# Kernel tuning notes

Measured on AMD Instinct MI355X. Metric: run time of the kernel, lower is better.

The kernel has to match this reference:

```python
import jax, jax.numpy as jnp
import numpy as np
from jax import lax

B, S, V, E, H, L, LAT = 32, 64, 32000, 128, 512, 2, 64

def setup_inputs() -> dict:
    key = jax.random.key(0)
    ks = jax.random.split(key, 40)
    sc = 0.05
    inputs = jax.random.randint(ks[0], (B, S), 0, V, dtype=jnp.int32)
    lengths = jnp.sort(jax.random.randint(ks[1], (B,), 1, S + 1, dtype=jnp.int32))[::-1]
    lengths = lengths.at[0].set(S)  # enforce_sorted=True, max length == S for static shapes
    d = {
        'inputs': inputs,
        'lengths': lengths,
        'noise': jax.random.normal(ks[2], (L, B, LAT), jnp.float32),
        'embed_table': jax.random.normal(ks[3], (V, E), jnp.float32) * sc,
        'enc_Wm': jax.random.normal(ks[4], (LAT, E), jnp.float32) * sc,
        'enc_bm': jnp.zeros((LAT,), jnp.float32),
        'enc_Wv': jax.random.normal(ks[5], (LAT, E), jnp.float32) * sc,
        'enc_bv': jnp.zeros((LAT,), jnp.float32),
        'W_l2r': jax.random.normal(ks[6], (H, LAT), jnp.float32) * sc,
        'b_l2r': jnp.zeros((H,), jnp.float32),
        'gru_Wih0': jax.random.normal(ks[7], (3 * H, E), jnp.float32) * sc,
        'gru_Whh0': jax.random.normal(ks[8], (3 * H, H), jnp.float32) * sc,
        'gru_bih0': jnp.zeros((3 * H,), jnp.float32),
        'gru_bhh0': jnp.zeros((3 * H,), jnp.float32),
        'gru_Wih1': jax.random.normal(ks[9], (3 * H, H), jnp.float32) * sc,
        'gru_Whh1': jax.random.normal(ks[10], (3 * H, H), jnp.float32) * sc,
        'gru_bih1': jnp.zeros((3 * H,), jnp.float32),
        'gru_bhh1': jnp.zeros((3 * H,), jnp.float32),
        'W_out': jax.random.normal(ks[11], (V, H), jnp.float32) * sc,
        'b_out': jnp.zeros((V,), jnp.float32),
        'logp_W1': jax.random.normal(ks[12], (200, LAT), jnp.float32) * sc,
        'logp_b1': jnp.zeros((200,), jnp.float32),
        'logp_W2': jax.random.normal(ks[13], (100, 200), jnp.float32) * sc,
        'logp_b2': jnp.zeros((100,), jnp.float32),
        'logp_W3': jax.random.normal(ks[14], (1, 100), jnp.float32) * sc,
        'logp_b3': jnp.zeros((1,), jnp.float32),
        'sas_W1': jax.random.normal(ks[15], (200, LAT), jnp.float32) * sc,
        'sas_b1': jnp.zeros((200,), jnp.float32),
        'sas_W2': jax.random.normal(ks[16], (100, 200), jnp.float32) * sc,
        'sas_b2': jnp.zeros((100,), jnp.float32),
        'sas_W3': jax.random.normal(ks[17], (1, 100), jnp.float32) * sc,
        'sas_b3': jnp.zeros((1,), jnp.float32),
    }
    return d

def _gru_layer(x, h0, Wih, Whh, bih, bhh, lengths):
    # x: [B,T,D]; PyTorch GRU gate order: r, z, n. Packed semantics: state frozen
    # and output zero beyond each sample's length.
    T = x.shape[1]
    xW = jnp.einsum('btd,gd->btg', x, Wih) + bih          # [B,T,3H] one big GEMM
    tmask = jnp.arange(T)[:, None] < lengths[None, :]      # [T,B]
    def step(h, inp):
        xw_t, m_t = inp                                    # [B,3H], [B]
        hW = h @ Whh.T + bhh
        xr, xz, xn = jnp.split(xw_t, 3, axis=-1)
        hr, hz, hn = jnp.split(hW, 3, axis=-1)
        r = jax.nn.sigmoid(xr + hr)
        u = jax.nn.sigmoid(xz + hz)
        n = jnp.tanh(xn + r * hn)
        h_new = (1.0 - u) * n + u * h
        m = m_t[:, None]
        h = jnp.where(m, h_new, h)
        out = jnp.where(m, h_new, 0.0)
        return h, out
    hT, outs = lax.scan(step, h0, (xW.transpose(1, 0, 2), tmask))
    return outs.transpose(1, 0, 2), hT                     # [B,T,H], [B,H]

def _mlp3(x, W1, b1, W2, b2, W3, b3):
    h = jax.nn.relu(x @ W1.T + b1)
    h = jax.nn.relu(h @ W2.T + b2)
    return (h @ W3.T + b3).reshape(-1)

def reference(inputs, lengths, noise, embed_table, enc_Wm, enc_bm, enc_Wv, enc_bv,
              W_l2r, b_l2r, gru_Wih0, gru_Whh0, gru_bih0, gru_bhh0,
              gru_Wih1, gru_Whh1, gru_bih1, gru_bhh1, W_out, b_out,
              logp_W1, logp_b1, logp_W2, logp_b2, logp_W3, logp_b3,
              sas_W1, sas_b1, sas_W2, sas_b2, sas_W3, sas_b3):
    emb = embed_table[inputs]                              # [B,S,E] gather
    # ragged masked segment-sum: sum embeddings of tokens with id > 2 per sample
    mask = (inputs > 2)[..., None].astype(emb.dtype)
    vec_frag = jnp.sum(emb * mask, axis=1)                 # [B,E]
    mean = vec_frag @ enc_Wm.T + enc_bm                    # [B,LAT]
    logv = vec_frag @ enc_Wv.T + enc_bv
    std = jnp.exp(0.5 * logv)
    z = noise * std + mean                                 # [L,B,LAT]
    pred_logp = _mlp3(mean, logp_W1, logp_b1, logp_W2, logp_b2, logp_W3, logp_b3)
    pred_sas = _mlp3(mean, sas_W1, sas_b1, sas_W2, sas_b2, sas_W3, sas_b3)
    state = z @ W_l2r.T + b_l2r                            # [L,B,H]
    # decoder: 2-layer GRU (eval mode: no dropout), then vocab projection
    out0, _ = _gru_layer(emb, state[0], gru_Wih0, gru_Whh0, gru_bih0, gru_bhh0, lengths)
    out1, _ = _gru_layer(out0, state[1], gru_Wih1, gru_Whh1, gru_bih1, gru_bhh1, lengths)
    output = out1 @ W_out.T + b_out                        # [B,S,V]
    return (output, mean, std, z, pred_logp, pred_sas)
```

## Files before the change

### kernel.cpp

```cpp
#include <hip/hip_runtime.h>


typedef __attribute__((ext_vector_type(8))) short bf16x8_t;
typedef __attribute__((ext_vector_type(8))) unsigned short u16x8_t;
typedef __attribute__((ext_vector_type(4))) float f32x4_t;
typedef __attribute__((ext_vector_type(8))) _Float16 f16x8_t;
typedef __attribute__((ext_vector_type(4))) unsigned int u32x4_t;

#define AS_AGENT __HIP_MEMORY_SCOPE_AGENT

static __device__ __forceinline__ unsigned short f2bf(float f) {
    unsigned int u = __float_as_uint(f);
    u += 0x7fffu + ((u >> 16) & 1u);
    return (unsigned short)(u >> 16);
}
static __device__ __forceinline__ unsigned short f2h(float f) {
    _Float16 h = (_Float16)f;
    return __builtin_bit_cast(unsigned short, h);
}
static __device__ __forceinline__ float sigmoidf_(float x) {
    return 1.f / (1.f + __expf(-x));
}

__global__ __launch_bounds__(256) void cvt_bf16_kernel(const float* __restrict__ in,
                                                       unsigned short* __restrict__ out, int n4) {
    int stride = gridDim.x * 256;
    for (int i = blockIdx.x * 256 + threadIdx.x; i < n4; i += stride) {
        float4 v = reinterpret_cast<const float4*>(in)[i];
        ushort4 o;
        o.x = f2bf(v.x); o.y = f2bf(v.y); o.z = f2bf(v.z); o.w = f2bf(v.w);
        reinterpret_cast<ushort4*>(out)[i] = o;
    }
}

__global__ __launch_bounds__(128) void embed_kernel(const int* __restrict__ tok,
                                                    const float* __restrict__ table,
                                                    unsigned short* __restrict__ embb,
                                                    float* __restrict__ vf) {
    const int b = blockIdx.x, e = threadIdx.x;
    float acc = 0.f;
    for (int s = 0; s < 64; ++s) {
        int id = tok[b * 64 + s];
        float v = table[(size_t)id * 128 + e];
        embb[(size_t)(b * 64 + s) * 128 + e] = f2bf(v);
        if (id > 2) acc += v;
    }
    vf[b * 128 + e] = acc;
}

__global__ __launch_bounds__(256) void encoder_kernel(
    const float* __restrict__ vf,
    const float* __restrict__ Wm, const float* __restrict__ bm,
    const float* __restrict__ Wv, const float* __restrict__ bv,
    const float* __restrict__ noise,
    const float* __restrict__ Wl2r, const float* __restrict__ bl2r,
    const float* __restrict__ lW1, const float* __restrict__ lb1,
    const float* __restrict__ lW2, const float* __restrict__ lb2,
    const float* __restrict__ lW3, const float* __restrict__ lb3,
    const float* __restrict__ sW1, const float* __restrict__ sb1,
    const float* __restrict__ sW2, const float* __restrict__ sb2,
    const float* __restrict__ sW3, const float* __restrict__ sb3,
    float* __restrict__ o_mean, float* __restrict__ o_std, float* __restrict__ o_z,
    float* __restrict__ o_logp, float* __restrict__ o_sas,
    float* __restrict__ state)
{
    const int b = blockIdx.x, tid = threadIdx.x;
    __shared__ float v_[128], mn[64], sd[64], zz[2][64], hh1[200], hh2[100];
    if (tid < 128) v_[tid] = vf[b * 128 + tid];
    __syncthreads();
    if (tid < 128) {
        int j = tid & 63;
        bool isv = tid >= 64;
        const float* W = (isv ? Wv : Wm) + j * 128;
        float a = isv ? bv[j] : bm[j];
#pragma unroll 4
        for (int k = 0; k < 128; ++k) a = fmaf(v_[k], W[k], a);
        if (!isv) { mn[j] = a; o_mean[b * 64 + j] = a; }
        else      { float s = __expf(0.5f * a); sd[j] = s; o_std[b * 64 + j] = s; }
    }
    __syncthreads();
    if (tid < 128) {
        int l = tid >> 6, j = tid & 63;
        float zv = fmaf(noise[(l * 32 + b) * 64 + j], sd[j], mn[j]);
        zz[l][j] = zv;
        o_z[(l * 32 + b) * 64 + j] = zv;
    }
    __syncthreads();
#pragma unroll
    for (int p = 0; p < 4; ++p) {
        int tt = p * 256 + tid;
        int l = tt >> 9, hd = tt & 511;
        const float* W = Wl2r + hd * 64;
        float a = bl2r[hd];
#pragma unroll 4
        for (int k = 0; k < 64; ++k) a = fmaf(zz[l][k], W[k], a);
        state[(size_t)(l * 32 + b) * 512 + hd] = a;
    }
    if (tid < 200) {
        const float* W = lW1 + tid * 64;
        float a = lb1[tid];
        for (int k = 0; k < 64; ++k) a = fmaf(mn[k], W[k], a);
        hh1[tid] = fmaxf(a, 0.f);
    }
    __syncthreads();
    if (tid < 100) {
        const float* W = lW2 + tid * 200;
        float a = lb2[tid];
        for (int k = 0; k < 200; ++k) a = fmaf(hh1[k], W[k], a);
        hh2[tid] = fmaxf(a, 0.f);
    }
    __syncthreads();
    if (tid == 0) {
        float a = lb3[0];
        for (int k = 0; k < 100; ++k) a = fmaf(hh2[k], lW3[k], a);
        o_logp[b] = a;
    }
    __syncthreads();
    if (tid < 200) {
        const float* W = sW1 + tid * 64;
        float a = sb1[tid];
        for (int k = 0; k < 64; ++k) a = fmaf(mn[k], W[k], a);
        hh1[tid] = fmaxf(a, 0.f);
    }
    __syncthreads();
    if (tid < 100) {
        const float* W = sW2 + tid * 200;
        float a = sb2[tid];
        for (int k = 0; k < 200; ++k) a = fmaf(hh1[k], W[k], a);
        hh2[tid] = fmaxf(a, 0.f);
    }
    __syncthreads();
    if (tid == 0) {
        float a = sb3[0];
        for (int k = 0; k < 100; ++k) a = fmaf(hh2[k], sW3[k], a);
        o_sas[b] = a;
    }
}

__global__ __launch_bounds__(256) void gemm_bt_kernel(
    const unsigned short* __restrict__ A,
    const unsigned short* __restrict__ B,
    const float* __restrict__ bias,
    float* __restrict__ C,
    int M, int N, int K)
{
    __shared__ unsigned short lA[128 * 64];
    __shared__ unsigned short lB[128 * 64];
    const int tid = threadIdx.x;
    const int lane = tid & 63;
    const int wave = tid >> 6;
    const int wm = wave >> 1, wn = wave & 1;
    const int m0 = blockIdx.y * 128, n0 = blockIdx.x * 128;

    f32x4_t acc[4][4];
#pragma unroll
    for (int i = 0; i < 4; ++i)
#pragma unroll
        for (int j = 0; j < 4; ++j) acc[i][j] = (f32x4_t){0.f, 0.f, 0.f, 0.f};

    for (int kt = 0; kt < K; kt += 64) {
#pragma unroll
        for (int p = 0; p < 4; ++p) {
            int g = p * 256 + tid;
            int row = g >> 3, c8 = g & 7;
            int dst = row * 64 + ((c8 ^ (row & 7)) << 3);
            *(u16x8_t*)&lA[dst] = *(const u16x8_t*)(A + (size_t)(m0 + row) * K + kt + (c8 << 3));
            *(u16x8_t*)&lB[dst] = *(const u16x8_t*)(B + (size_t)(n0 + row) * K + kt + (c8 << 3));
        }
        __syncthreads();
#pragma unroll
        for (int kc = 0; kc < 2; ++kc) {
            bf16x8_t af[4], bfr[4];
            int c8 = kc * 4 + (lane >> 4);
#pragma unroll
            for (int i = 0; i < 4; ++i) {
                int ra = wm * 64 + i * 16 + (lane & 15);
                af[i] = *(const bf16x8_t*)&lA[ra * 64 + ((c8 ^ (ra & 7)) << 3)];
                int rb = wn * 64 + i * 16 + (lane & 15);
                bfr[i] = *(const bf16x8_t*)&lB[rb * 64 + ((c8 ^ (rb & 7)) << 3)];
            }
#pragma unroll
            for (int i = 0; i < 4; ++i)
#pragma unroll
                for (int j = 0; j < 4; ++j)
                    acc[i][j] = __builtin_amdgcn_mfma_f32_16x16x32_bf16(af[i], bfr[j], acc[i][j], 0, 0, 0);
        }
        __syncthreads();
    }
    const int lm = (lane >> 4) * 4, ln = lane & 15;
#pragma unroll
    for (int i = 0; i < 4; ++i) {
        int gm = m0 + wm * 64 + i * 16 + lm;
#pragma unroll
        for (int j = 0; j < 4; ++j) {
            int gn = n0 + wn * 64 + j * 16 + ln;
            float bb = bias ? bias[gn] : 0.f;
#pragma unroll
            for (int r = 0; r < 4; ++r)
                C[(size_t)(gm + r) * N + gn] = acc[i][j][r] + bb;
        }
    }
}

#define NWG_L0 16
#define NWG_TOT 48
#define NWG_ALL 256
#define NWG_GEMM 208

__global__ __launch_bounds__(512) void gru_fused_kernel(
    const float* __restrict__ xW0,
    const float* __restrict__ Whh0, const float* __restrict__ bhh0,
    const float* __restrict__ Whh1, const float* __restrict__ Wih1,
    const float* __restrict__ bih1, const float* __restrict__ bhh1,
    const float* __restrict__ hinit,
    const int* __restrict__ lengths,
    unsigned short* __restrict__ h0x,
    unsigned short* __restrict__ h1x,
    unsigned short* __restrict__ o0x,
    unsigned short* __restrict__ out1x,
    const unsigned short* __restrict__ Woutb,
    const float* __restrict__ bout,
    float* __restrict__ outp,
    int* __restrict__ flags)
{
    __shared__ __align__(16) char smem[157184];
    const int tid = threadIdx.x;
    const int wg = blockIdx.x;
    const int lane = tid & 63;
    const int wave = tid >> 6;
    unsigned int* __restrict__ h0x32 = (unsigned int*)h0x;
    unsigned int* __restrict__ h1x32 = (unsigned int*)h1x;
    unsigned int* __restrict__ o0x32 = (unsigned int*)o0x;
    unsigned int* __restrict__ o1x32 = (unsigned int*)out1x;

    if (wg >= NWG_TOT) {
        unsigned short* lA = (unsigned short*)smem;
        unsigned short* lB = (unsigned short*)(smem + 16384);
        const int g = wg - NWG_TOT;
        const int wm = wave >> 2;
        const int wn = wave & 3;
        int mPrev = -1;
        for (int T = g; T < 4000; T += NWG_GEMM) {
            const int m = T / 250, n = T % 250;
            if (m != mPrev) {
                if (wave == 0) {
                    const int tgt = 4 * m + 6;
                    for (;;) {
                        int v = 0x40000000;
                        if (lane < 32)
                            v = __hip_atomic_load(&flags[(NWG_L0 + lane) << 5],
                                                  __ATOMIC_RELAXED, AS_AGENT);
                        if (__all(v >= tgt)) break;
                        __builtin_amdgcn_s_sleep(8);
                    }
                }
                __syncthreads();
                mPrev = m;
            }
            f32x4_t acc[4][2];
#pragma unroll
            for (int i = 0; i < 4; ++i)
#pragma unroll
                for (int j = 0; j < 2; ++j) acc[i][j] = (f32x4_t){0.f, 0.f, 0.f, 0.f};

            for (int kt = 0; kt < 512; kt += 64) {
#pragma unroll
                for (int p = 0; p < 2; ++p) {
                    int gi = p * 512 + tid;
                    int row = gi >> 3, c8 = gi & 7;
                    int dst = row * 64 + ((c8 ^ (row & 7)) << 3);
                    u32x4_t qa, qb;
                    const char* srcA = (const char*)out1x +
                        (((size_t)(m * 128 + row)) * 512 + kt + (c8 << 3)) * 2;
                    const char* srcB = (const char*)Woutb +
                        (((size_t)(n * 128 + row)) * 512 + kt + (c8 << 3)) * 2;
                    asm volatile("global_load_dwordx4 %0, %1, off sc0 sc1"
                                 : "=v"(qa) : "v"(srcA) : "memory");
                    asm volatile("global_load_dwordx4 %0, %1, off"
                                 : "=v"(qb) : "v"(srcB) : "memory");
                    asm volatile("s_waitcnt vmcnt(0)" ::: "memory");
                    *(u32x4_t*)&lA[dst] = qa;
                    *(u32x4_t*)&lB[dst] = qb;
                }
                __syncthreads();
#pragma unroll
                for (int kc = 0; kc < 2; ++kc) {
                    bf16x8_t af[4], bfr[2];
                    int c8 = kc * 4 + (lane >> 4);
#pragma unroll
                    for (int i = 0; i < 4; ++i) {
                        int ra = wm * 64 + i * 16 + (lane & 15);
                        af[i] = *(const bf16x8_t*)&lA[ra * 64 + ((c8 ^ (ra & 7)) << 3)];
                    }
#pragma unroll
                    for (int j = 0; j < 2; ++j) {
                        int rb = wn * 32 + j * 16 + (lane & 15);
                        bfr[j] = *(const bf16x8_t*)&lB[rb * 64 + ((c8 ^ (rb & 7)) << 3)];
                    }
#pragma unroll
                    for (int i = 0; i < 4; ++i)
#pragma unroll
                        for (int j = 0; j < 2; ++j)
                            acc[i][j] = __builtin_amdgcn_mfma_f32_16x16x32_bf16(
                                af[i], bfr[j], acc[i][j], 0, 0, 0);
                }
                __syncthreads();
            }
            const int lm = (lane >> 4) * 4, ln = lane & 15;
#pragma unroll
            for (int i = 0; i < 4; ++i) {
                int rl0 = wm * 64 + i * 16 + lm;
#pragma unroll
                for (int j = 0; j < 2; ++j) {
                    int gn = n * 128 + wn * 32 + j * 16 + ln;
                    float bb = bout[gn];
#pragma unroll
                    for (int r = 0; r < 4; ++r) {
                        int rl = rl0 + r;
                        int t = 4 * m + (rl >> 5), b = rl & 31;
                        outp[(size_t)(b * 64 + t) * 32000 + gn] = acc[i][j][r] + bb;
                    }
                }
            }
        }
        return;
    }

    unsigned short* Wl = (unsigned short*)smem;
    u32x4_t* hstage4 = (u32x4_t*)(smem + 98304);
    float* csm = (float*)(smem + 131072);
#define CSM(p, gt, b, c) csm[((((p)*3 + (gt)) * 32 + (b)) * 34) + (c)]
    const int gate = wave >> 1;
    const int mt = wave & 1;

    if (wg < NWG_L0) {
        const int d0 = wg * 32;
        for (int idx = tid; idx < 6144; idx += 512) {
            int ln = idx & 63, kk = (idx >> 6) & 15, nt = (idx >> 10) & 1, g_ = idx >> 11;
            int grow = g_ * 512 + d0 + nt * 16 + (ln & 15);
            int k = kk * 32 + ((ln >> 4) << 3);
            const float* src = Whh0 + (size_t)grow * 512 + k;
            f16x8_t v;
#pragma unroll
            for (int j = 0; j < 8; ++j) v[j] = (_Float16)src[j];
            *(f16x8_t*)&Wl[idx << 3] = v;
        }
        const int ub = tid >> 4, dpl = (tid & 15) * 2, ud = d0 + dpl;
        float h_lo = hinit[(size_t)ub * 512 + ud];
        float h_hi = hinit[(size_t)ub * 512 + ud + 1];
        const float br_lo = bhh0[ud],        br_hi = bhh0[ud + 1];
        const float bz_lo = bhh0[512 + ud],  bz_hi = bhh0[512 + ud + 1];
        const float bn_lo = bhh0[1024 + ud], bn_hi = bhh0[1024 + ud + 1];
        const int lenb = lengths[ub];
        {
            unsigned int hw = (unsigned int)f2h(h_lo) | ((unsigned int)f2h(h_hi) << 16);
            __hip_atomic_store(&h0x32[ub * 256 + (ud >> 1)], hw, __ATOMIC_RELAXED, AS_AGENT);
        }
        asm volatile("s_waitcnt vmcnt(0)" ::: "memory");
        __syncthreads();
        if (tid == 0) __hip_atomic_store(&flags[wg << 5], 1, __ATOMIC_RELAXED, AS_AGENT);
        const float* xrow = xW0 + (size_t)(ub * 64) * 1536 + ud;
        float2 px_r = *(const float2*)(xrow);
        float2 px_z = *(const float2*)(xrow + 512);
        float2 px_n = *(const float2*)(xrow + 1024);

        for (int r = 0; r < 64; ++r) {
            if (wave == 0) {
                const int tgt = r + 1;
                for (;;) {
                    int v = 0x40000000;
                    if (lane < NWG_TOT)
                        v = __hip_atomic_load(&flags[lane << 5], __ATOMIC_RELAXED, AS_AGENT);
                    if (__all(v >= tgt)) break;
                    __builtin_amdgcn_s_sleep(1);
                }
            }
            __syncthreads();
            {
                const char* srcb = (const char*)h0x + ((r & 1) << 15);
                u32x4_t q0, q1, q2, q3;
                asm volatile("global_load_dwordx4 %0, %1, off sc0 sc1"
                             : "=v"(q0) : "v"(srcb + ((size_t)tid << 4)) : "memory");
                asm volatile("global_load_dwordx4 %0, %1, off sc0 sc1"
                             : "=v"(q1) : "v"(srcb + ((size_t)(512 + tid) << 4)) : "memory");
                asm volatile("global_load_dwordx4 %0, %1, off sc0 sc1"
                             : "=v"(q2) : "v"(srcb + ((size_t)(1024 + tid) << 4)) : "memory");
                asm volatile("global_load_dwordx4 %0, %1, off sc0 sc1"
                             : "=v"(q3) : "v"(srcb + ((size_t)(1536 + tid) << 4)) : "memory");
                asm volatile("s_waitcnt vmcnt(0)" ::: "memory");
                int g0 = tid, g1 = 512 + tid, g2 = 1024 + tid, g3 = 1536 + tid;
                hstage4[g0 ^ ((g0 >> 6) & 7)] = q0;
                hstage4[g1 ^ ((g1 >> 6) & 7)] = q1;
                hstage4[g2 ^ ((g2 >> 6) & 7)] = q2;
                hstage4[g3 ^ ((g3 >> 6) & 7)] = q3;
            }
            __syncthreads();
            if (wave < 6) {
                const int brow = mt * 16 + (lane & 15);
                const int ko = lane >> 4;
                f32x4_t acc0 = (f32x4_t){0.f, 0.f, 0.f, 0.f};
                f32x4_t acc1 = (f32x4_t){0.f, 0.f, 0.f, 0.f};
#pragma unroll
                for (int kk = 0; kk < 16; ++kk) {
                    int gg = brow * 64 + kk * 4 + ko;
                    f16x8_t af = __builtin_bit_cast(f16x8_t, hstage4[gg ^ (brow & 7)]);
                    f16x8_t bf0 = *(const f16x8_t*)&Wl[(((gate * 2 + 0) * 16 + kk) * 64 + lane) << 3];
                    f16x8_t bf1 = *(const f16x8_t*)&Wl[(((gate * 2 + 1) * 16 + kk) * 64 + lane) << 3];
                    acc0 = __builtin_amdgcn_mfma_f32_16x16x32_f16(af, bf0, acc0, 0, 0, 0);
                    acc1 = __builtin_amdgcn_mfma_f32_16x16x32_f16(af, bf1, acc1, 0, 0, 0);
                }
                const int crow = mt * 16 + ((lane >> 4) << 2), ccol = lane & 15;
#pragma unroll
                for (int rr = 0; rr < 4; ++rr) {
                    CSM(0, gate, crow + rr, ccol) = acc0[rr];
                    CSM(0, gate, crow + rr, 16 + ccol) = acc1[rr];
                }
            }
            __syncthreads();
            unsigned int ow = 0u;
            if (r < lenb) {
                float hr_lo = CSM(0, 0, ub, dpl), hr_hi = CSM(0, 0, ub, dpl + 1);
                float hz_lo = CSM(0, 1, ub, dpl), hz_hi = CSM(0, 1, ub, dpl + 1);
                float hn_lo = CSM(0, 2, ub, dpl), hn_hi = CSM(0, 2, ub, dpl + 1);
                float r0 = sigmoidf_(px_r.x + hr_lo + br_lo);
                float r1 = sigmoidf_(px_r.y + hr_hi + br_hi);
                float u0 = sigmoidf_(px_z.x + hz_lo + bz_lo);
                float u1 = sigmoidf_(px_z.y + hz_hi + bz_hi);
                float n0 = tanhf(px_n.x + r0 * (hn_lo + bn_lo));
                float n1 = tanhf(px_n.y + r1 * (hn_hi + bn_hi));
                h_lo = (1.f - u0) * n0 + u0 * h_lo;
                h_hi = (1.f - u1) * n1 + u1 * h_hi;
                ow = (unsigned int)f2h(h_lo) | ((unsigned int)f2h(h_hi) << 16);
            }
            {
                unsigned int hw = (unsigned int)f2h(h_lo) | ((unsigned int)f2h(h_hi) << 16);
                __hip_atomic_store(&h0x32[((r + 1) & 1) * 8192 + ub * 256 + (ud >> 1)],
                                   hw, __ATOMIC_RELAXED, AS_AGENT);
                __hip_atomic_store(&o0x32[(r & 1) * 8192 + ub * 256 + (ud >> 1)],
                                   ow, __ATOMIC_RELAXED, AS_AGENT);
            }
            asm volatile("s_waitcnt vmcnt(0)" ::: "memory");
            __syncthreads();
            if (tid == 0) __hip_atomic_store(&flags[wg << 5], r + 2, __ATOMIC_RELAXED, AS_AGENT);
            {
                int tn = r + 1 < 64 ? r + 1 : 63;
                const float* xp = xW0 + (size_t)(ub * 64 + tn) * 1536 + ud;
                px_r = *(const float2*)(xp);
                px_z = *(const float2*)(xp + 512);
                px_n = *(const float2*)(xp + 1024);
            }
        }
    } else {
        const int lid = wg - NWG_L0;
        const int d0 = lid * 16;
        for (int idx = tid; idx < 6144; idx += 512) {
            int ln = idx & 63, kk = (idx >> 6) & 31, g_ = idx >> 11;
            int grow = g_ * 512 + d0 + (ln & 15);
            int k = (kk & 15) * 32 + ((ln >> 4) << 3);
            const float* src = (kk < 16 ? Whh1 : Wih1) + (size_t)grow * 512 + k;
            f16x8_t v;
#pragma unroll
            for (int j = 0; j < 8; ++j) v[j] = (_Float16)src[j];
            *(f16x8_t*)&Wl[idx << 3] = v;
        }
        const bool upd = (tid < 256);
        const int ub = tid >> 3, dpl = (tid & 7) * 2, ud = d0 + dpl;
        float h_lo = 0.f, h_hi = 0.f;
        float br_lo = 0.f, br_hi = 0.f, bz_lo = 0.f, bz_hi = 0.f;
        float bxn_lo = 0.f, bxn_hi = 0.f, bhn_lo = 0.f, bhn_hi = 0.f;
        int lenb = 0;
        if (upd) {
            h_lo = hinit[16384 + (size_t)ub * 512 + ud];
            h_hi = hinit[16384 + (size_t)ub * 512 + ud + 1];
            br_lo = bih1[ud] + bhh1[ud];
            br_hi = bih1[ud + 1] + bhh1[ud + 1];
            bz_lo = bih1[512 + ud] + bhh1[512 + ud];
            bz_hi = bih1[512 + ud + 1] + bhh1[512 + ud + 1];
            bxn_lo = bih1[1024 + ud];   bxn_hi = bih1[1024 + ud + 1];
            bhn_lo = bhh1[1024 + ud];   bhn_hi = bhh1[1024 + ud + 1];
            lenb = lengths[ub];
            unsigned int hw = (unsigned int)f2h(h_lo) | ((unsigned int)f2h(h_hi) << 16);
            __hip_atomic_store(&h1x32[8192 + ub * 256 + (ud >> 1)], hw, __ATOMIC_RELAXED, AS_AGENT);
        }
        asm volatile("s_waitcnt vmcnt(0)" ::: "memory");
        __syncthreads();
        if (tid == 0) __hip_atomic_store(&flags[wg << 5], 2, __ATOMIC_RELAXED, AS_AGENT);

        for (int r = 1; r <= 64; ++r) {
            const int t1 = r - 1;
            if (wave == 0) {
                const int tgt = r + 1;
                for (;;) {
                    int v = 0x40000000;
                    if (lane < NWG_TOT)
                        v = __hip_atomic_load(&flags[lane << 5], __ATOMIC_RELAXED, AS_AGENT);
                    if (__all(v >= tgt)) break;
                    __builtin_amdgcn_s_sleep(1);
                }
            }
            __syncthreads();
            u32x4_t a0, a1, a2, a3, b0, b1, b2, b3;
            {
                const char* sh = (const char*)h1x + ((r & 1) << 15);
                const char* so = (const char*)o0x + (((r + 1) & 1) << 15);
                asm volatile("global_load_dwordx4 %0, %1, off sc0 sc1"
                             : "=v"(a0) : "v"(sh + ((size_t)tid << 4)) : "memory");
                asm volatile("global_load_dwordx4 %0, %1, off sc0 sc1"
                             : "=v"(a1) : "v"(sh + ((size_t)(512 + tid) << 4)) : "memory");
                asm volatile("global_load_dwordx4 %0, %1, off sc0 sc1"
                             : "=v"(a2) : "v"(sh + ((size_t)(1024 + tid) << 4)) : "memory");
                asm volatile("global_load_dwordx4 %0, %1, off sc0 sc1"
                             : "=v"(a3) : "v"(sh + ((size_t)(1536 + tid) << 4)) : "memory");
                asm volatile("global_load_dwordx4 %0, %1, off sc0 sc1"
                             : "=v"(b0) : "v"(so + ((size_t)tid << 4)) : "memory");
                asm volatile("global_load_dwordx4 %0, %1, off sc0 sc1"
                             : "=v"(b1) : "v"(so + ((size_t)(512 + tid) << 4)) : "memory");
                asm volatile("global_load_dwordx4 %0, %1, off sc0 sc1"
                             : "=v"(b2) : "v"(so + ((size_t)(1024 + tid) << 4)) : "memory");
                asm volatile("global_load_dwordx4 %0, %1, off sc0 sc1"
                             : "=v"(b3) : "v"(so + ((size_t)(1536 + tid) << 4)) : "memory");
                asm volatile("s_waitcnt vmcnt(4)" ::: "memory");
                int g0 = tid, g1 = 512 + tid, g2 = 1024 + tid, g3 = 1536 + tid;
                hstage4[g0 ^ ((g0 >> 6) & 7)] = a0;
                hstage4[g1 ^ ((g1 >> 6) & 7)] = a1;
                hstage4[g2 ^ ((g2 >> 6) & 7)] = a2;
                hstage4[g3 ^ ((g3 >> 6) & 7)] = a3;
            }
            __syncthreads();
            f32x4_t acc_h = (f32x4_t){0.f, 0.f, 0.f, 0.f};
            const int brow = mt * 16 + (lane & 15);
            const int ko = lane >> 4;
            if (wave < 6) {
#pragma unroll
                for (int kk = 0; kk < 16; ++kk) {
                    int gg = brow * 64 + kk * 4 + ko;
                    f16x8_t af = __builtin_bit_cast(f16x8_t, hstage4[gg ^ (brow & 7)]);
                    f16x8_t bf = *(const f16x8_t*)&Wl[(((gate * 32 + kk) * 64 + lane)) << 3];
                    acc_h = __builtin_amdgcn_mfma_f32_16x16x32_f16(af, bf, acc_h, 0, 0, 0);
                }
            }
            __syncthreads();
            {
                asm volatile("s_waitcnt vmcnt(0)" ::: "memory");
                int g0 = tid, g1 = 512 + tid, g2 = 1024 + tid, g3 = 1536 + tid;
                hstage4[g0 ^ ((g0 >> 6) & 7)] = b0;
                hstage4[g1 ^ ((g1 >> 6) & 7)] = b1;
                hstage4[g2 ^ ((g2 >> 6) & 7)] = b2;
                hstage4[g3 ^ ((g3 >> 6) & 7)] = b3;
            }
            __syncthreads();
            if (wave < 6) {
                f32x4_t acc_x = (f32x4_t){0.f, 0.f, 0.f, 0.f};
#pragma unroll
                for (int kk = 0; kk < 16; ++kk) {
                    int gg = brow * 64 + kk * 4 + ko;
                    f16x8_t af = __builtin_bit_cast(f16x8_t, hstage4[gg ^ (brow & 7)]);
                    f16x8_t bf = *(const f16x8_t*)&Wl[(((gate * 32 + 16 + kk) * 64 + lane)) << 3];
                    acc_x = __builtin_amdgcn_mfma_f32_16x16x32_f16(af, bf, acc_x, 0, 0, 0);
                }
                const int crow = mt * 16 + ((lane >> 4) << 2), ccol = lane & 15;
#pragma unroll
                for (int rr = 0; rr < 4; ++rr) {
                    CSM(0, gate, crow + rr, ccol) = acc_h[rr];
                    CSM(1, gate, crow + rr, ccol) = acc_x[rr];
                }
            }
            __syncthreads();
            unsigned int ow = 0u;
            if (upd) {
                if (t1 < lenb) {
                    float hr_lo = CSM(0, 0, ub, dpl), hr_hi = CSM(0, 0, ub, dpl + 1);
                    float hz_lo = CSM(0, 1, ub, dpl), hz_hi = CSM(0, 1, ub, dpl + 1);
                    float hn_lo = CSM(0, 2, ub, dpl), hn_hi = CSM(0, 2, ub, dpl + 1);
                    float xr_lo = CSM(1, 0, ub, dpl), xr_hi = CSM(1, 0, ub, dpl + 1);
                    float xz_lo = CSM(1, 1, ub, dpl), xz_hi = CSM(1, 1, ub, dpl + 1);
                    float xn_lo = CSM(1, 2, ub, dpl), xn_hi = CSM(1, 2, ub, dpl + 1);
                    float r0 = sigmoidf_(xr_lo + hr_lo + br_lo);
                    float r1 = sigmoidf_(xr_hi + hr_hi + br_hi);
                    float u0 = sigmoidf_(xz_lo + hz_lo + bz_lo);
                    float u1 = sigmoidf_(xz_hi + hz_hi + bz_hi);
                    float n0 = tanhf(xn_lo + bxn_lo + r0 * (hn_lo + bhn_lo));
                    float n1 = tanhf(xn_hi + bxn_hi + r1 * (hn_hi + bhn_hi));
                    h_lo = (1.f - u0) * n0 + u0 * h_lo;
                    h_hi = (1.f - u1) * n1 + u1 * h_hi;
                    ow = (unsigned int)f2bf(h_lo) | ((unsigned int)f2bf(h_hi) << 16);
                }
                if (r < 64) {
                    unsigned int hw = (unsigned int)f2h(h_lo) | ((unsigned int)f2h(h_hi) << 16);
                    __hip_atomic_store(&h1x32[((r + 1) & 1) * 8192 + ub * 256 + (ud >> 1)],
                                       hw, __ATOMIC_RELAXED, AS_AGENT);
                }
                __hip_atomic_store(&o1x32[(size_t)(t1 * 32 + ub) * 256 + (ud >> 1)],
                                   ow, __ATOMIC_RELAXED, AS_AGENT);
            }
            asm volatile("s_waitcnt vmcnt(0)" ::: "memory");
            __syncthreads();
            if (tid == 0)
                __hip_atomic_store(&flags[wg << 5], r + 2, __ATOMIC_RELAXED, AS_AGENT);
        }
    }
#undef CSM
}

extern "C" void kernel_launch(void* const* d_in, const int* in_sizes, int n_in,
                              void* d_out, int out_size, void* d_ws, size_t ws_size,
                              hipStream_t stream) {
    const int*   tok    = (const int*)d_in[0];
    const int*   lens   = (const int*)d_in[1];
    const float* noise  = (const float*)d_in[2];
    const float* table  = (const float*)d_in[3];
    const float* Wm     = (const float*)d_in[4];
    const float* bm_    = (const float*)d_in[5];
    const float* Wv     = (const float*)d_in[6];
    const float* bv_    = (const float*)d_in[7];
    const float* Wl2r   = (const float*)d_in[8];
    const float* bl2r   = (const float*)d_in[9];
    const float* Wih0   = (const float*)d_in[10];
    const float* Whh0   = (const float*)d_in[11];
    const float* bih0   = (const float*)d_in[12];
    const float* bhh0   = (const float*)d_in[13];
    const float* Wih1   = (const float*)d_in[14];
    const float* Whh1   = (const float*)d_in[15];
    const float* bih1   = (const float*)d_in[16];
    const float* bhh1   = (const float*)d_in[17];
    const float* Wout   = (const float*)d_in[18];
    const float* bout   = (const float*)d_in[19];
    const float* lW1 = (const float*)d_in[20]; const float* lb1 = (const float*)d_in[21];
    const float* lW2 = (const float*)d_in[22]; const float* lb2 = (const float*)d_in[23];
    const float* lW3 = (const float*)d_in[24]; const float* lb3 = (const float*)d_in[25];
    const float* sW1 = (const float*)d_in[26]; const float* sb1 = (const float*)d_in[27];
    const float* sW2 = (const float*)d_in[28]; const float* sb2 = (const float*)d_in[29];
    const float* sW3 = (const float*)d_in[30]; const float* sb3 = (const float*)d_in[31];

    float* out    = (float*)d_out;
    float* o_mean = out + 65536000;
    float* o_std  = o_mean + 2048;
    float* o_z    = o_std + 2048;
    float* o_logp = o_z + 4096;
    float* o_sas  = o_logp + 32;

    char* ws = (char*)d_ws;
    unsigned short* Woutb = (unsigned short*)ws;  ws += 32768000;
    unsigned short* Wih0b = (unsigned short*)ws;  ws += 393216;
    unsigned short* embb  = (unsigned short*)ws;  ws += 524288;
    float*          vf    = (float*)ws;           ws += 16384;
    float*          state = (float*)ws;           ws += 131072;
    float*          xW    = (float*)ws;           ws += 12582912;
    unsigned short* out1x = (unsigned short*)ws;  ws += 2097152;
    unsigned short* h0x   = (unsigned short*)ws;  ws += 131072;
    unsigned short* h1x   = (unsigned short*)ws;  ws += 131072;
    unsigned short* o0x   = (unsigned short*)ws;  ws += 131072;
    int*            flgp  = (int*)ws;             ws += 8192;

    cvt_bf16_kernel<<<dim3(4096), dim3(256), 0, stream>>>(Wout, Woutb, 16384000 / 4);
    cvt_bf16_kernel<<<dim3(192),  dim3(256), 0, stream>>>(Wih0, Wih0b, 196608 / 4);
    hipMemsetAsync(flgp, 0, 8192, stream);

    embed_kernel<<<dim3(32), dim3(128), 0, stream>>>(tok, table, embb, vf);
    encoder_kernel<<<dim3(32), dim3(256), 0, stream>>>(vf, Wm, bm_, Wv, bv_, noise, Wl2r, bl2r,
                                                       lW1, lb1, lW2, lb2, lW3, lb3,
                                                       sW1, sb1, sW2, sb2, sW3, sb3,
                                                       o_mean, o_std, o_z, o_logp, o_sas, state);

    gemm_bt_kernel<<<dim3(12, 16), dim3(256), 0, stream>>>(embb, Wih0b, bih0, xW, 2048, 1536, 128);
    gru_fused_kernel<<<dim3(NWG_ALL), dim3(512), 0, stream>>>(
        xW, Whh0, bhh0, Whh1, Wih1, bih1, bhh1, state, lens,
        h0x, h1x, o0x, out1x, Woutb, bout, out, flgp);
}
```

Before: 377.5 us.

## Overlap W_out bf16 conversion with GRU recurrence inside fused kernel

The standalone W_out fp32-to-bf16 conversion kernel is removed. Its work now runs inside the idle GEMM workgroups of the fused GRU kernel, overlapping the recurrent layers, and a flag barrier among those workgroups follows. The embed, encoder and Wih0 conversion kernels are merged into one launch, cutting launches and an intermediate buffer. out1x is padded per 4-timestep chunk and the inline-asm cache-bypassing loads become plain loads. This risks stale-cache reads and competes for bandwidth with the recurrent workgroups.

```diff
diff --git a/kernel.cpp b/kernel.cpp
--- a/kernel.cpp
+++ b/kernel.cpp
@@ -22,34 +22,9 @@
     return 1.f / (1.f + __expf(-x));
 }
 
-__global__ __launch_bounds__(256) void cvt_bf16_kernel(const float* __restrict__ in,
-                                                       unsigned short* __restrict__ out, int n4) {
-    int stride = gridDim.x * 256;
-    for (int i = blockIdx.x * 256 + threadIdx.x; i < n4; i += stride) {
-        float4 v = reinterpret_cast<const float4*>(in)[i];
-        ushort4 o;
-        o.x = f2bf(v.x); o.y = f2bf(v.y); o.z = f2bf(v.z); o.w = f2bf(v.w);
-        reinterpret_cast<ushort4*>(out)[i] = o;
-    }
-}
-
-__global__ __launch_bounds__(128) void embed_kernel(const int* __restrict__ tok,
-                                                    const float* __restrict__ table,
-                                                    unsigned short* __restrict__ embb,
-                                                    float* __restrict__ vf) {
-    const int b = blockIdx.x, e = threadIdx.x;
-    float acc = 0.f;
-    for (int s = 0; s < 64; ++s) {
-        int id = tok[b * 64 + s];
-        float v = table[(size_t)id * 128 + e];
-        embb[(size_t)(b * 64 + s) * 128 + e] = f2bf(v);
-        if (id > 2) acc += v;
-    }
-    vf[b * 128 + e] = acc;
-}
-
-__global__ __launch_bounds__(256) void encoder_kernel(
-    const float* __restrict__ vf,
+__global__ __launch_bounds__(256) void embed_encoder_kernel(
+    const int* __restrict__ tok, const float* __restrict__ table,
+    const float* __restrict__ Wih0f,
     const float* __restrict__ Wm, const float* __restrict__ bm,
     const float* __restrict__ Wv, const float* __restrict__ bv,
     const float* __restrict__ noise,
@@ -62,11 +37,29 @@
     const float* __restrict__ sW3, const float* __restrict__ sb3,
     float* __restrict__ o_mean, float* __restrict__ o_std, float* __restrict__ o_z,
     float* __restrict__ o_logp, float* __restrict__ o_sas,
-    float* __restrict__ state)
+    float* __restrict__ state,
+    unsigned short* __restrict__ embb,
+    unsigned short* __restrict__ Wih0b)
 {
     const int b = blockIdx.x, tid = threadIdx.x;
     __shared__ float v_[128], mn[64], sd[64], zz[2][64], hh1[200], hh2[100];
-    if (tid < 128) v_[tid] = vf[b * 128 + tid];
+    if (tid < 128) {
+        const int e = tid;
+        float acc = 0.f;
+        for (int s = 0; s < 64; ++s) {
+            int id = tok[b * 64 + s];
+            float v = table[(size_t)id * 128 + e];
+            embb[(size_t)(b * 64 + s) * 128 + e] = f2bf(v);
+            if (id > 2) acc += v;
+        }
+        v_[e] = acc;
+    }
+    for (int i = b * 256 + tid; i < 49152; i += 8192) {
+        float4 v = reinterpret_cast<const float4*>(Wih0f)[i];
+        ushort4 o;
+        o.x = f2bf(v.x); o.y = f2bf(v.y); o.z = f2bf(v.z); o.w = f2bf(v.w);
+        reinterpret_cast<ushort4*>(Wih0b)[i] = o;
+    }
     __syncthreads();
     if (tid < 128) {
         int j = tid & 63;
@@ -206,6 +199,7 @@
 #define NWG_TOT 48
 #define NWG_ALL 256
 #define NWG_GEMM 208
+#define OCH 32832
 
 __global__ __launch_bounds__(512) void gru_fused_kernel(
     const float* __restrict__ xW0,
@@ -218,7 +212,8 @@
     unsigned short* __restrict__ h1x,
     unsigned short* __restrict__ o0x,
     unsigned short* __restrict__ out1x,
-    const unsigned short* __restrict__ Woutb,
+    const float* __restrict__ Woutf,
+    unsigned short* __restrict__ Woutb,
     const float* __restrict__ bout,
     float* __restrict__ outp,
     int* __restrict__ flags)
@@ -233,12 +228,43 @@
     unsigned int* __restrict__ o0x32 = (unsigned int*)o0x;
     unsigned int* __restrict__ o1x32 = (unsigned int*)out1x;
 
+    (void)__hip_atomic_load(&flags[0], __ATOMIC_ACQUIRE, AS_AGENT);
+
     if (wg >= NWG_TOT) {
         unsigned short* lA = (unsigned short*)smem;
         unsigned short* lB = (unsigned short*)(smem + 16384);
         const int g = wg - NWG_TOT;
         const int wm = wave >> 2;
         const int wn = wave & 3;
+
+        for (int i = g * 512 + tid; i < 4096000; i += NWG_GEMM * 512) {
+            float4 v = reinterpret_cast<const float4*>(Woutf)[i];
+            unsigned int lo = (unsigned int)f2bf(v.x) | ((unsigned int)f2bf(v.y) << 16);
+            unsigned int hi = (unsigned int)f2bf(v.z) | ((unsigned int)f2bf(v.w) << 16);
+            unsigned long long w = (unsigned long long)lo | ((unsigned long long)hi << 32);
+            __hip_atomic_store((unsigned long long*)Woutb + i, w, __ATOMIC_RELAXED, AS_AGENT);
+        }
+        asm volatile("s_waitcnt vmcnt(0)" ::: "memory");
+        __syncthreads();
+        if (tid == 0) __hip_atomic_store(&flags[wg << 5], 1, __ATOMIC_RELAXED, AS_AGENT);
+        if (wave == 0) {
+            for (;;) {
+                int mn = 1;
+#pragma unroll
+                for (int j = 0; j < 4; ++j) {
+                    int idx = lane * 4 + j;
+                    if (idx < NWG_GEMM) {
+                        int v = __hip_atomic_load(&flags[(NWG_TOT + idx) << 5],
+                                                  __ATOMIC_RELAXED, AS_AGENT);
+                        mn = v < mn ? v : mn;
+                    }
+                }
+                if (__all(mn >= 1)) break;
+                __builtin_amdgcn_s_sleep(8);
+            }
+        }
+        __syncthreads();
+
         int mPrev = -1;
         for (int T = g; T < 4000; T += NWG_GEMM) {
             const int m = T / 250, n = T % 250;
@@ -269,16 +295,10 @@
                     int gi = p * 512 + tid;
                     int row = gi >> 3, c8 = gi & 7;
                     int dst = row * 64 + ((c8 ^ (row & 7)) << 3);
-                    u32x4_t qa, qb;
-                    const char* srcA = (const char*)out1x +
-                        (((size_t)(m * 128 + row)) * 512 + kt + (c8 << 3)) * 2;
-                    const char* srcB = (const char*)Woutb +
-                        (((size_t)(n * 128 + row)) * 512 + kt + (c8 << 3)) * 2;
-                    asm volatile("global_load_dwordx4 %0, %1, off sc0 sc1"
-                                 : "=v"(qa) : "v"(srcA) : "memory");
-                    asm volatile("global_load_dwordx4 %0, %1, off"
-                                 : "=v"(qb) : "v"(srcB) : "memory");
-                    asm volatile("s_waitcnt vmcnt(0)" ::: "memory");
+                    u32x4_t qa = *(const u32x4_t*)(out1x + (size_t)m * 65664 +
+                                                   row * 512 + kt + (c8 << 3));
+                    u32x4_t qb = *(const u32x4_t*)(Woutb + ((size_t)(n * 128 + row)) * 512 +
+                                                   kt + (c8 << 3));
                     *(u32x4_t*)&lA[dst] = qa;
                     *(u32x4_t*)&lB[dst] = qb;
                 }
@@ -590,7 +610,8 @@
                     __hip_atomic_store(&h1x32[((r + 1) & 1) * 8192 + ub * 256 + (ud >> 1)],
                                        hw, __ATOMIC_RELAXED, AS_AGENT);
                 }
-                __hip_atomic_store(&o1x32[(size_t)(t1 * 32 + ub) * 256 + (ud >> 1)],
+                __hip_atomic_store(&o1x32[(size_t)(t1 >> 2) * OCH +
+                                          ((t1 & 3) * 32 + ub) * 256 + (ud >> 1)],
                                    ow, __ATOMIC_RELAXED, AS_AGENT);
             }
             asm volatile("s_waitcnt vmcnt(0)" ::: "memory");
@@ -643,27 +664,23 @@
     unsigned short* Woutb = (unsigned short*)ws;  ws += 32768000;
     unsigned short* Wih0b = (unsigned short*)ws;  ws += 393216;
     unsigned short* embb  = (unsigned short*)ws;  ws += 524288;
-    float*          vf    = (float*)ws;           ws += 16384;
     float*          state = (float*)ws;           ws += 131072;
     float*          xW    = (float*)ws;           ws += 12582912;
-    unsigned short* out1x = (unsigned short*)ws;  ws += 2097152;
+    unsigned short* out1x = (unsigned short*)ws;  ws += 2101248;
     unsigned short* h0x   = (unsigned short*)ws;  ws += 131072;
     unsigned short* h1x   = (unsigned short*)ws;  ws += 131072;
     unsigned short* o0x   = (unsigned short*)ws;  ws += 131072;
-    int*            flgp  = (int*)ws;             ws += 8192;
-
-    cvt_bf16_kernel<<<dim3(4096), dim3(256), 0, stream>>>(Wout, Woutb, 16384000 / 4);
-    cvt_bf16_kernel<<<dim3(192),  dim3(256), 0, stream>>>(Wih0, Wih0b, 196608 / 4);
-    hipMemsetAsync(flgp, 0, 8192, stream);
-
-    embed_kernel<<<dim3(32), dim3(128), 0, stream>>>(tok, table, embb, vf);
-    encoder_kernel<<<dim3(32), dim3(256), 0, stream>>>(vf, Wm, bm_, Wv, bv_, noise, Wl2r, bl2r,
-                                                       lW1, lb1, lW2, lb2, lW3, lb3,
-                                                       sW1, sb1, sW2, sb2, sW3, sb3,
-                                                       o_mean, o_std, o_z, o_logp, o_sas, state);
+    int*            flgp  = (int*)ws;             ws += 32768;
+
+    (void)hipMemsetAsync(flgp, 0, 32768, stream);
+
+    embed_encoder_kernel<<<dim3(32), dim3(256), 0, stream>>>(
+        tok, table, Wih0, Wm, bm_, Wv, bv_, noise, Wl2r, bl2r,
+        lW1, lb1, lW2, lb2, lW3, lb3, sW1, sb1, sW2, sb2, sW3, sb3,
+        o_mean, o_std, o_z, o_logp, o_sas, state, embb, Wih0b);
 
     gemm_bt_kernel<<<dim3(12, 16), dim3(256), 0, stream>>>(embb, Wih0b, bih0, xW, 2048, 1536, 128);
     gru_fused_kernel<<<dim3(NWG_ALL), dim3(512), 0, stream>>>(
         xW, Whh0, bhh0, Whh1, Wih1, bih1, bhh1, state, lens,
-        h0x, h1x, o0x, out1x, Woutb, bout, out, flgp);
+        h0x, h1x, o0x, out1x, Wout, Woutb, bout, out, flgp);
 }
```

Result: no change. 380.2 us (+0.7%).
